# Kernel tuning notes

Hardware: AMD Instinct MI355X
Metric: run time of the kernel (lower is better)

The kernel has to match this reference:

```python
import jax, jax.numpy as jnp
import numpy as np

BS, SL, N_AGENTS, OBS_DIM, STATE_DIM, N_EDGES, HID = 32, 512, 32, 96, 1024, 64, 256


def _hgcn(w_line, x, H):
    # x: [B, n, 1]; H: [B, n, E]. Faithful to torch HGCN:
    # A = D^{-1/2} H |W| B^{-1} H^T D^{-1/2}, with D, B built from detached H/|W|,
    # inf entries (from 0^{-1} / 0^{-0.5}) zeroed. Diagonal matmuls are implicit scalings.
    w_abs = jnp.abs(w_line)
    Hd = jax.lax.stop_gradient(H)
    d = jnp.einsum('bne,e->bn', Hd, jax.lax.stop_gradient(w_abs))  # [B, n]
    d_is = jnp.where(d > 0, jax.lax.rsqrt(jnp.where(d > 0, d, 1.0)), 0.0)
    b = jnp.sum(Hd, axis=-2)  # [B, E]
    b_inv = jnp.where(b > 0, 1.0 / jnp.where(b > 0, b, 1.0), 0.0)
    t = d_is[..., None] * x                       # D^{-1/2} x
    s = jnp.einsum('bne,bnk->bek', H, t)          # H^T (...)
    s = s * (w_abs[None, :] * b_inv)[..., None]   # |W| B^{-1} (diagonals commute)
    y = jnp.einsum('bne,bek->bnk', H, s)          # H (...)
    return d_is[..., None] * y                    # D^{-1/2} (...)


def _mlp(x, w1, b1, w2, b2):
    return jax.nn.relu(x @ w1 + b1) @ w2 + b2


def setup_inputs() -> dict:
    key = jax.random.key(0)
    ks = jax.random.split(key, 24)
    f = jax.random.normal
    inp = {
        'agent_qs': f(ks[0], (BS, SL, N_AGENTS), jnp.float32),
        'states': f(ks[1], (BS, SL, STATE_DIM), jnp.float32),
        'indiv_us': f(ks[2], (BS, SL, N_AGENTS, OBS_DIM), jnp.float32),
        'edge_W': f(ks[3], (OBS_DIM, N_EDGES), jnp.float32) * 0.1,
        'edge_b': f(ks[4], (N_EDGES,), jnp.float32) * 0.1,
        'wline1': 1.0 + 0.1 * f(ks[5], (N_EDGES,), jnp.float32),
        'wline2': 1.0 + 0.1 * f(ks[6], (N_EDGES,), jnp.float32),
    }
    names = ['hw1', 'hc1', 'hw', 'hc']
    outs = [N_AGENTS, N_AGENTS, N_AGENTS, 1]
    for i, (nm, od) in enumerate(zip(names, outs)):
        inp[nm + '_w1'] = f(ks[7 + 4 * i], (STATE_DIM, HID), jnp.float32) * 0.05
        inp[nm + '_b1'] = f(ks[8 + 4 * i], (HID,), jnp.float32) * 0.05
        inp[nm + '_w2'] = f(ks[9 + 4 * i], (HID, od), jnp.float32) * 0.05
        inp[nm + '_b2'] = f(ks[10 + 4 * i], (od,), jnp.float32) * 0.05
    return inp


def reference(agent_qs, states, indiv_us, edge_W, edge_b, wline1, wline2,
              hw1_w1, hw1_b1, hw1_w2, hw1_b2, hc1_w1, hc1_b1, hc1_w2, hc1_b2,
              hw_w1, hw_b1, hw_w2, hw_b2, hc_w1, hc_b1, hc_w2, hc_b2):
    bs, sl, n = agent_qs.shape
    q = agent_qs.reshape(-1, n)                               # [B, n]
    u = indiv_us.reshape(-1, n, indiv_us.shape[-1])           # [B, n, obs]
    s = states.reshape(-1, states.shape[-1])                  # [B, state_dim]
    H = jax.nn.relu(u @ edge_W + edge_b)                      # hyper_edge_net -> [B, n, E]
    x = q[..., None]                                          # node_features [B, n, 1]
    qs_tot = _hgcn(wline2, _hgcn(wline1, x, H), H)[..., 0]    # two stacked HGCN encoders
    w1 = jnp.abs(_mlp(s, hw1_w1, hw1_b1, hw1_w2, hw1_b2))
    c1 = _mlp(s, hc1_w1, hc1_b1, hc1_w2, hc1_b2)
    qt = jax.nn.elu(qs_tot * w1 + c1)
    w = jnp.abs(_mlp(s, hw_w1, hw_b1, hw_w2, hw_b2))
    c = _mlp(s, hc_w1, hc_b1, hc_w2, hc_b2)[..., 0]
    q_tot = jnp.sum(qt * w, axis=-1) + c
    return q_tot.reshape(bs, sl, 1)
```

## Files before the change

kernel.cpp:

```cpp
#include <hip/hip_runtime.h>
#include <cstdint>

typedef _Float16 f16;
typedef _Float16 f16x2 __attribute__((ext_vector_type(2)));
typedef _Float16 f16x4 __attribute__((ext_vector_type(4)));
typedef _Float16 f16x8 __attribute__((ext_vector_type(8)));
typedef float f32x4 __attribute__((ext_vector_type(4)));

#define AS1U const __attribute__((address_space(1))) unsigned int
#define AS3U __attribute__((address_space(3))) unsigned int

__device__ __forceinline__ void gload_lds16(const void* g, void* l) {
    __builtin_amdgcn_global_load_lds((AS1U*)g, (AS3U*)l, 16, 0, 0);
}

#define WSYNC() asm volatile("s_waitcnt lgkmcnt(0)" ::: "memory")
#define CFENCE() asm volatile("" ::: "memory")

#define BATCH 16384
#define NAG   32
#define OBS   96
#define SDIM  1024
#define NE    64
#define HIDN  256
#define NH    1024

#define NB_MIX 5120
#define NB_PW  256
#define NB_SM  101
#define NB_MAIN (NB_MIX + NB_PW + NB_SM)

__global__ __launch_bounds__(256, 5) void k_main(
    const float* __restrict__ agent_qs, const float* __restrict__ states,
    const float* __restrict__ indiv_us, const float* __restrict__ edge_W,
    const float* __restrict__ edge_b, const float* __restrict__ wline1,
    const float* __restrict__ wline2,
    const float* __restrict__ w1a, const float* __restrict__ w1b,
    const float* __restrict__ w1c, const float* __restrict__ w1d,
    const float* __restrict__ b1a, const float* __restrict__ b1b,
    const float* __restrict__ b1c, const float* __restrict__ b1d,
    const float* __restrict__ w2a, const float* __restrict__ w2b,
    const float* __restrict__ w2c, const float* __restrict__ w2d,
    f16* __restrict__ states16, f16* __restrict__ W1t, float* __restrict__ b1cat,
    f16* __restrict__ W2t, f16* __restrict__ hcw2, float* __restrict__ qs_tot) {
    __shared__ __align__(16) char arena[32256];
    const int tid = threadIdx.x;
    int bid = blockIdx.x;

    if (bid < NB_MIX) {
        const int g = bid / 5, r = bid - g * 5;
        if (r == 4) {
            int i = g * 256 + tid;
            const int n4 = BATCH * SDIM / 4;
            const int stride = 1024 * 256;
            for (; i < n4; i += stride) {
                float4 v = ((const float4*)states)[i];
                f16x4 h = { (f16)v.x, (f16)v.y, (f16)v.z, (f16)v.w };
                ((f16x4*)states16)[i] = h;
            }
            return;
        }
        const int hbid = g * 4 + r;
        f16*   eWs  = (f16*)arena;
        float* swa  = (float*)(arena + 13312);
        f16*   HsB  = (f16*)(arena + 13824);
        float* svB  = (float*)(arena + 30720);
        float* sttB = (float*)(arena + 31744);

        const int w = tid >> 6, l = tid & 63;
        const int b = hbid * 4 + w;
        f16*   Hw  = HsB + w * (32 * 66);
        float* sv  = svB + w * 64;
        float* stt = sttB + w * 32;

        const int nn = l & 31, half = l >> 5;
        float q = agent_qs[(size_t)b * 32 + nn];

        for (int i = tid; i < 6144; i += 256) {
            int k = i >> 6, n = i & 63;
            eWs[n * 104 + k] = (f16)edge_W[i];
        }
        if (tid < 64) swa[tid] = fabsf(wline1[tid]);
        else if (tid < 128) swa[tid] = fabsf(wline2[tid - 64]);
        __syncthreads();

        const float swal1 = swa[l];
        const float swal2 = swa[64 + l];

        const int lm = l & 15, lk = l >> 4;
        const float* ub = indiv_us + (size_t)b * (NAG * OBS);

        #pragma unroll
        for (int mt = 0; mt < 2; mt++) {
            f16x8 af[3];
            #pragma unroll
            for (int ks = 0; ks < 3; ks++) {
                const float* up = ub + (mt * 16 + lm) * 96 + ks * 32 + lk * 8;
                float4 v0 = *(const float4*)up;
                float4 v1 = *(const float4*)(up + 4);
                af[ks] = (f16x8){ (f16)v0.x, (f16)v0.y, (f16)v0.z, (f16)v0.w,
                                  (f16)v1.x, (f16)v1.y, (f16)v1.z, (f16)v1.w };
            }
            #pragma unroll
            for (int nt = 0; nt < 4; nt++) {
                f32x4 acc = {0.f, 0.f, 0.f, 0.f};
                #pragma unroll
                for (int ks = 0; ks < 3; ks++) {
                    f16x8 bb = *(const f16x8*)&eWs[(nt * 16 + lm) * 104 + ks * 32 + lk * 8];
                    acc = __builtin_amdgcn_mfma_f32_16x16x32_f16(af[ks], bb, acc, 0, 0, 0);
                }
                int col = nt * 16 + lm;
                float bias = edge_b[col];
                #pragma unroll
                for (int r2 = 0; r2 < 4; r2++) {
                    int row = mt * 16 + lk * 4 + r2;
                    float hv = acc[r2] + bias;
                    Hw[row * 66 + col] = (f16)(hv > 0.f ? hv : 0.f);
                }
            }
        }
        WSYNC();

        float bsum = 0.f;
        #pragma unroll
        for (int n = 0; n < 32; n++) bsum += (float)Hw[n * 66 + l];
        const float sbinv_r = bsum > 0.f ? 1.f / bsum : 0.f;

        float dd = 0.f;
        #pragma unroll 8
        for (int e2 = 0; e2 < 32; e2++) {
            f16x2 h2 = *(const f16x2*)&Hw[nn * 66 + e2 * 2];
            dd += (float)h2.x * swa[half * 64 + e2 * 2] + (float)h2.y * swa[half * 64 + e2 * 2 + 1];
        }
        float dis = dd > 0.f ? rsqrtf(dd) : 0.f;
        const float dis_o = __shfl_xor(dis, 32);
        const float dis1 = (half == 0) ? dis : dis_o;
        const float dis2 = (half == 0) ? dis_o : dis;
        if (half == 0) stt[nn] = dis * q;
        WSYNC();

        float s1 = 0.f;
        #pragma unroll
        for (int n = 0; n < 32; n++) s1 += (float)Hw[n * 66 + l] * stt[n];
        sv[l] = s1 * swal1 * sbinv_r;
        WSYNC();

        float y1 = 0.f;
        #pragma unroll 8
        for (int e2 = 0; e2 < 32; e2++) {
            f16x2 h2 = *(const f16x2*)&Hw[nn * 66 + e2 * 2];
            y1 += (float)h2.x * sv[e2 * 2] + (float)h2.y * sv[e2 * 2 + 1];
        }
        float x2 = dis1 * y1;
        if (half == 0) stt[nn] = dis2 * x2;
        WSYNC();

        float s2 = 0.f;
        #pragma unroll
        for (int n = 0; n < 32; n++) s2 += (float)Hw[n * 66 + l] * stt[n];
        sv[l] = s2 * swal2 * sbinv_r;
        WSYNC();

        float y2 = 0.f;
        #pragma unroll 8
        for (int e2 = 0; e2 < 32; e2++) {
            f16x2 h2 = *(const f16x2*)&Hw[nn * 66 + e2 * 2];
            y2 += (float)h2.x * sv[e2 * 2] + (float)h2.y * sv[e2 * 2 + 1];
        }
        if (half == 0) qs_tot[(size_t)b * 32 + nn] = dis2 * y2;
        return;
    }
    bid -= NB_MIX;

    if (bid < NB_PW) {
        float* tile = (float*)arena;
        int mlp = bid >> 6, rem = bid & 63, kt = rem >> 2, ct = rem & 3;
        const float* src = (mlp == 0) ? w1a : (mlp == 1) ? w1b : (mlp == 2) ? w1c : w1d;
        int k0 = kt * 64, c0 = ct * 64;
        for (int i = tid; i < 4096; i += 256) {
            int kk = i >> 6, cc = i & 63;
            tile[kk * 65 + cc] = src[(size_t)(k0 + kk) * 256 + c0 + cc];
        }
        __syncthreads();
        for (int i = tid; i < 4096; i += 256) {
            int cc = i >> 6, kk = i & 63;
            W1t[(size_t)(mlp * 256 + c0 + cc) * 1024 + k0 + kk] = (f16)tile[kk * 65 + cc];
        }
        return;
    }
    bid -= NB_PW;
    {
        int i = bid * 256 + tid;
        if (i < 24576) {
            int mp = i >> 13, rem = i & 8191, oo = rem >> 8, kk = rem & 255;
            const float* src = (mp == 0) ? w2a : (mp == 1) ? w2b : w2c;
            W2t[i] = (f16)src[kk * 32 + oo];
        } else if (i < 24832) {
            int k = i - 24576;
            hcw2[k] = (f16)w2d[k];
        } else if (i < 25856) {
            int n = i - 24832;
            int mlp = n >> 8, c = n & 255;
            const float* bsrc = (mlp == 0) ? b1a : (mlp == 1) ? b1b : (mlp == 2) ? b1c : b1d;
            b1cat[n] = bsrc[c];
        }
    }
}

__global__ __launch_bounds__(512) void k_gemm(
    const f16* __restrict__ A, const f16* __restrict__ B,
    const float* __restrict__ b1cat, const f16* __restrict__ W2t,
    const f16* __restrict__ hcw2, float* __restrict__ Pp) {
    __shared__ __align__(16) char smem[131072];
    f16* Asb = (f16*)smem;
    f16* Bsb = (f16*)(smem + 65536);
    f16* Ts  = (f16*)smem;

    const int tid = threadIdx.x;
    const int w = tid >> 6, l = tid & 63;
    const int lm = l & 15, lk = l >> 4;
    const int wm = w >> 2, wn = w & 3;
    const int p = blockIdx.x;
    const int xcd = p & 7, s = p >> 3;
    const int mt = xcd * 8 + (s >> 2);
    const int nt = s & 3;
    const int m0 = mt * 256, n0 = nt * 256;
    const int c0 = w * 4;
    const int srow = l >> 3;
    const int gchunk = (l & 7) ^ srow;

    float bj[4];
    #pragma unroll
    for (int j = 0; j < 4; j++) bj[j] = b1cat[n0 + wn * 64 + j * 16 + lm];

    f32x4 acc[8][4];
    #pragma unroll
    for (int i = 0; i < 8; i++)
        #pragma unroll
        for (int j = 0; j < 4; j++) acc[i][j] = (f32x4){0.f, 0.f, 0.f, 0.f};

#define STAGE(KT, BI)                                                                     \
    {                                                                                     \
        f16* Ad = Asb + (BI) * 16384;                                                     \
        f16* Bd = Bsb + (BI) * 16384;                                                     \
        _Pragma("unroll")                                                                 \
        for (int i_ = 0; i_ < 4; i_++) {                                                  \
            int cc = c0 + i_;                                                             \
            gload_lds16(&A[(size_t)(m0 + cc * 8 + srow) * 1024 + (KT) * 64 + gchunk * 8], \
                        &Ad[cc * 512]);                                                   \
            gload_lds16(&B[(size_t)(n0 + cc * 8 + srow) * 1024 + (KT) * 64 + gchunk * 8], \
                        &Bd[cc * 512]);                                                   \
        }                                                                                 \
    }

    STAGE(0, 0);
    STAGE(1, 1);

    for (int kt = 0; kt < 16; kt++) {
        if (kt < 15) { asm volatile("s_waitcnt vmcnt(8)" ::: "memory"); }
        else         { asm volatile("s_waitcnt vmcnt(0)" ::: "memory"); }
        CFENCE(); __builtin_amdgcn_s_barrier(); CFENCE();

        const f16* As_ = Asb + (kt & 1) * 16384;
        const f16* Bs_ = Bsb + (kt & 1) * 16384;
        const int swlo = ((lk ^ (lm & 7)) << 3);
        const int swhi = (((4 + lk) ^ (lm & 7)) << 3);

        f16x8 af[4][2], bf01[2][2], bf23[2][2];

        #pragma unroll
        for (int i = 0; i < 4; i++) {
            af[i][0] = *(const f16x8*)&As_[(wm * 128 + i * 16 + lm) * 64 + swlo];
            af[i][1] = *(const f16x8*)&As_[(wm * 128 + i * 16 + lm) * 64 + swhi];
        }
        #pragma unroll
        for (int j = 0; j < 2; j++) {
            bf01[j][0] = *(const f16x8*)&Bs_[(wn * 64 + j * 16 + lm) * 64 + swlo];
            bf01[j][1] = *(const f16x8*)&Bs_[(wn * 64 + j * 16 + lm) * 64 + swhi];
        }
        __builtin_amdgcn_s_setprio(1);
        #pragma unroll
        for (int ks = 0; ks < 2; ks++)
            #pragma unroll
            for (int i = 0; i < 4; i++)
                #pragma unroll
                for (int j = 0; j < 2; j++)
                    acc[i][j] = __builtin_amdgcn_mfma_f32_16x16x32_f16(af[i][ks], bf01[j][ks], acc[i][j], 0, 0, 0);
        __builtin_amdgcn_s_setprio(0);
        CFENCE(); __builtin_amdgcn_s_barrier(); CFENCE();

        #pragma unroll
        for (int j = 0; j < 2; j++) {
            bf23[j][0] = *(const f16x8*)&Bs_[(wn * 64 + (2 + j) * 16 + lm) * 64 + swlo];
            bf23[j][1] = *(const f16x8*)&Bs_[(wn * 64 + (2 + j) * 16 + lm) * 64 + swhi];
        }
        __builtin_amdgcn_s_setprio(1);
        #pragma unroll
        for (int ks = 0; ks < 2; ks++)
            #pragma unroll
            for (int i = 0; i < 4; i++)
                #pragma unroll
                for (int j = 0; j < 2; j++)
                    acc[i][2 + j] = __builtin_amdgcn_mfma_f32_16x16x32_f16(af[i][ks], bf23[j][ks], acc[i][2 + j], 0, 0, 0);
        __builtin_amdgcn_s_setprio(0);
        CFENCE(); __builtin_amdgcn_s_barrier(); CFENCE();

        #pragma unroll
        for (int i = 0; i < 4; i++) {
            af[i][0] = *(const f16x8*)&As_[(wm * 128 + (4 + i) * 16 + lm) * 64 + swlo];
            af[i][1] = *(const f16x8*)&As_[(wm * 128 + (4 + i) * 16 + lm) * 64 + swhi];
        }
        __builtin_amdgcn_s_setprio(1);
        #pragma unroll
        for (int ks = 0; ks < 2; ks++)
            #pragma unroll
            for (int i = 0; i < 4; i++)
                #pragma unroll
                for (int j = 0; j < 2; j++)
                    acc[4 + i][j] = __builtin_amdgcn_mfma_f32_16x16x32_f16(af[i][ks], bf01[j][ks], acc[4 + i][j], 0, 0, 0);
        __builtin_amdgcn_s_setprio(0);
        CFENCE(); __builtin_amdgcn_s_barrier(); CFENCE();

        if (kt < 14) STAGE(kt + 2, kt & 1);
        __builtin_amdgcn_s_setprio(1);
        #pragma unroll
        for (int ks = 0; ks < 2; ks++)
            #pragma unroll
            for (int i = 0; i < 4; i++)
                #pragma unroll
                for (int j = 0; j < 2; j++)
                    acc[4 + i][2 + j] = __builtin_amdgcn_mfma_f32_16x16x32_f16(af[i][ks], bf23[j][ks], acc[4 + i][2 + j], 0, 0, 0);
        __builtin_amdgcn_s_setprio(0);
    }
#undef STAGE

    __syncthreads();

    const int mlp = nt;
    #pragma unroll
    for (int pass = 0; pass < 2; pass++) {
        if (wm == pass) {
            #pragma unroll
            for (int i = 0; i < 8; i++)
                #pragma unroll
                for (int r = 0; r < 4; r++) {
                    int rl = i * 16 + lk * 4 + r;
                    #pragma unroll
                    for (int j = 0; j < 4; j++) {
                        float v = acc[i][j][r] + bj[j];
                        Ts[rl * 264 + wn * 64 + j * 16 + lm] = (f16)(v > 0.f ? v : 0.f);
                    }
                }
        }
        __syncthreads();
        const int grow = m0 + pass * 128 + w * 16;
        if (mlp < 3) {
            const f16* wb = W2t + mlp * 8192;
            f32x4 acc2[2];
            acc2[0] = (f32x4){0, 0, 0, 0}; acc2[1] = (f32x4){0, 0, 0, 0};
            #pragma unroll
            for (int ks = 0; ks < 8; ks++) {
                f16x8 a  = *(const f16x8*)&Ts[(w * 16 + lm) * 264 + ks * 32 + lk * 8];
                f16x8 b0 = *(const f16x8*)&wb[lm * 256 + ks * 32 + lk * 8];
                f16x8 b1 = *(const f16x8*)&wb[(16 + lm) * 256 + ks * 32 + lk * 8];
                acc2[0] = __builtin_amdgcn_mfma_f32_16x16x32_f16(a, b0, acc2[0], 0, 0, 0);
                acc2[1] = __builtin_amdgcn_mfma_f32_16x16x32_f16(a, b1, acc2[1], 0, 0, 0);
            }
            #pragma unroll
            for (int j2 = 0; j2 < 2; j2++)
                #pragma unroll
                for (int r = 0; r < 4; r++)
                    Pp[(size_t)(grow + lk * 4 + r) * 104 + mlp * 32 + j2 * 16 + lm] = acc2[j2][r];
        } else {
            f32x4 acc2 = (f32x4){0, 0, 0, 0};
            #pragma unroll
            for (int ks = 0; ks < 8; ks++) {
                f16x8 a = *(const f16x8*)&Ts[(w * 16 + lm) * 264 + ks * 32 + lk * 8];
                f16x8 bz = (f16x8){0, 0, 0, 0, 0, 0, 0, 0};
                if (lm == 0) bz = *(const f16x8*)&hcw2[ks * 32 + lk * 8];
                acc2 = __builtin_amdgcn_mfma_f32_16x16x32_f16(a, bz, acc2, 0, 0, 0);
            }
            if (lm == 0)
                #pragma unroll
                for (int r = 0; r < 4; r++)
                    Pp[(size_t)(grow + lk * 4 + r) * 104 + 96] = acc2[r];
        }
        if (pass == 0) __syncthreads();
    }
}

__global__ __launch_bounds__(256) void k_ep(
    const float* __restrict__ Pp, const float* __restrict__ qs_tot,
    const float* __restrict__ hw1_b2, const float* __restrict__ hc1_b2,
    const float* __restrict__ hw_b2, const float* __restrict__ hc_b2,
    float* __restrict__ out) {
    const int tid = threadIdx.x;
    const int row = blockIdx.x * 32 + (tid >> 3);
    const int q8 = tid & 7, o = q8 * 4;
    const float* p0 = Pp + (size_t)row * 104;
    f32x4 a0 = *(const f32x4*)(p0 + o);
    f32x4 c0 = *(const f32x4*)(p0 + 32 + o);
    f32x4 w0 = *(const f32x4*)(p0 + 64 + o);
    f32x4 qs = *(const f32x4*)(qs_tot + (size_t)row * 32 + o);
    float val = 0.f;
    #pragma unroll
    for (int j = 0; j < 4; j++) {
        float wv1 = fabsf(a0[j] + hw1_b2[o + j]);
        float cv1 = c0[j] + hc1_b2[o + j];
        float wv  = fabsf(w0[j] + hw_b2[o + j]);
        float z = qs[j] * wv1 + cv1;
        float qt = z > 0.f ? z : expm1f(z);
        val += qt * wv;
    }
    val += __shfl_xor(val, 1);
    val += __shfl_xor(val, 2);
    val += __shfl_xor(val, 4);
    if (q8 == 0) out[row] = val + p0[96] + hc_b2[0];
}

extern "C" void kernel_launch(void* const* d_in, const int* in_sizes, int n_in,
                              void* d_out, int out_size, void* d_ws, size_t ws_size,
                              hipStream_t stream) {
    const float* agent_qs = (const float*)d_in[0];
    const float* states   = (const float*)d_in[1];
    const float* indiv_us = (const float*)d_in[2];
    const float* edge_W   = (const float*)d_in[3];
    const float* edge_b   = (const float*)d_in[4];
    const float* wline1   = (const float*)d_in[5];
    const float* wline2   = (const float*)d_in[6];
    const float* hw1_w1 = (const float*)d_in[7];
    const float* hw1_b1 = (const float*)d_in[8];
    const float* hw1_w2 = (const float*)d_in[9];
    const float* hw1_b2 = (const float*)d_in[10];
    const float* hc1_w1 = (const float*)d_in[11];
    const float* hc1_b1 = (const float*)d_in[12];
    const float* hc1_w2 = (const float*)d_in[13];
    const float* hc1_b2 = (const float*)d_in[14];
    const float* hw_w1  = (const float*)d_in[15];
    const float* hw_b1  = (const float*)d_in[16];
    const float* hw_w2  = (const float*)d_in[17];
    const float* hw_b2  = (const float*)d_in[18];
    const float* hc_w1  = (const float*)d_in[19];
    const float* hc_b1  = (const float*)d_in[20];
    const float* hc_w2  = (const float*)d_in[21];
    const float* hc_b2  = (const float*)d_in[22];

    char* ws = (char*)d_ws;
    size_t o_states16 = 0;
    size_t o_W1t  = o_states16 + (size_t)BATCH * SDIM * 2;
    size_t o_b1   = o_W1t + (size_t)NH * SDIM * 2;
    size_t o_W2t  = o_b1 + 4096;
    size_t o_hcw2 = o_W2t + 49152;
    size_t o_Pp   = o_hcw2 + 512;
    size_t o_qs   = o_Pp + (size_t)BATCH * 104 * 4;

    f16*   states16 = (f16*)(ws + o_states16);
    f16*   W1t      = (f16*)(ws + o_W1t);
    float* b1cat    = (float*)(ws + o_b1);
    f16*   W2t      = (f16*)(ws + o_W2t);
    f16*   hcw2     = (f16*)(ws + o_hcw2);
    float* Pp       = (float*)(ws + o_Pp);
    float* qs_tot   = (float*)(ws + o_qs);

    k_main<<<NB_MAIN, 256, 0, stream>>>(
        agent_qs, states, indiv_us, edge_W, edge_b, wline1, wline2,
        hw1_w1, hc1_w1, hw_w1, hc_w1, hw1_b1, hc1_b1, hw_b1, hc_b1,
        hw1_w2, hc1_w2, hw_w2, hc_w2,
        states16, W1t, b1cat, W2t, hcw2, qs_tot);
    k_gemm<<<256, 512, 0, stream>>>(states16, W1t, b1cat, W2t, hcw2, Pp);
    k_ep<<<BATCH / 32, 256, 0, stream>>>(Pp, qs_tot, hw1_b2, hc1_b2, hw_b2, hc_b2,
                                         (float*)d_out);
}
```

Before: 116.6 us.

## Keep hypergraph incidence matrix in MFMA registers and reduce with wave shuffles

The HGCN part no longer writes the relu'd incidence matrix H to LDS in f16. It keeps the MFMA accumulator fragments in registers as fp32 and does the degree sums, the two H^T/H products and the normalisations with cross-lane xor-shuffle reductions. This removes the per-wave LDS traffic and the lgkmcnt waits, and shrinks the shared arena, which can allow more blocks per CU. The trade is many shuffle instructions and higher register pressure. The min-blocks hint is also dropped from launch_bounds, so the compiler may pick a different occupancy.

```diff
diff --git a/kernel.cpp b/kernel.cpp
--- a/kernel.cpp
+++ b/kernel.cpp
@@ -14,7 +14,6 @@
     __builtin_amdgcn_global_load_lds((AS1U*)g, (AS3U*)l, 16, 0, 0);
 }
 
-#define WSYNC() asm volatile("s_waitcnt lgkmcnt(0)" ::: "memory")
 #define CFENCE() asm volatile("" ::: "memory")
 
 #define BATCH 16384
@@ -30,7 +29,7 @@
 #define NB_SM  101
 #define NB_MAIN (NB_MIX + NB_PW + NB_SM)
 
-__global__ __launch_bounds__(256, 5) void k_main(
+__global__ __launch_bounds__(256) void k_main(
     const float* __restrict__ agent_qs, const float* __restrict__ states,
     const float* __restrict__ indiv_us, const float* __restrict__ edge_W,
     const float* __restrict__ edge_b, const float* __restrict__ wline1,
@@ -43,13 +42,13 @@
     const float* __restrict__ w2c, const float* __restrict__ w2d,
     f16* __restrict__ states16, f16* __restrict__ W1t, float* __restrict__ b1cat,
     f16* __restrict__ W2t, f16* __restrict__ hcw2, float* __restrict__ qs_tot) {
-    __shared__ __align__(16) char arena[32256];
+    __shared__ __align__(16) char arena[16640];
     const int tid = threadIdx.x;
     int bid = blockIdx.x;
 
     if (bid < NB_MIX) {
-        const int g = bid / 5, r = bid - g * 5;
-        if (r == 4) {
+        const int g = bid / 5, r5 = bid - g * 5;
+        if (r5 == 4) {
             int i = g * 256 + tid;
             const int n4 = BATCH * SDIM / 4;
             const int stride = 1024 * 256;
@@ -60,21 +59,13 @@
             }
             return;
         }
-        const int hbid = g * 4 + r;
-        f16*   eWs  = (f16*)arena;
-        float* swa  = (float*)(arena + 13312);
-        f16*   HsB  = (f16*)(arena + 13824);
-        float* svB  = (float*)(arena + 30720);
-        float* sttB = (float*)(arena + 31744);
+        const int hbid = g * 4 + r5;
+        f16*   eWs = (f16*)arena;
+        float* swa = (float*)(arena + 13312);
 
         const int w = tid >> 6, l = tid & 63;
         const int b = hbid * 4 + w;
-        f16*   Hw  = HsB + w * (32 * 66);
-        float* sv  = svB + w * 64;
-        float* stt = sttB + w * 32;
-
-        const int nn = l & 31, half = l >> 5;
-        float q = agent_qs[(size_t)b * 32 + nn];
+        const int lm = l & 15, lk = l >> 4;
 
         for (int i = tid; i < 6144; i += 256) {
             int k = i >> 6, n = i & 63;
@@ -84,12 +75,16 @@
         else if (tid < 128) swa[tid] = fabsf(wline2[tid - 64]);
         __syncthreads();
 
-        const float swal1 = swa[l];
-        const float swal2 = swa[64 + l];
-
-        const int lm = l & 15, lk = l >> 4;
+        float sw1[4], sw2[4], eb[4];
+        #pragma unroll
+        for (int nt = 0; nt < 4; nt++) {
+            sw1[nt] = swa[nt * 16 + lm];
+            sw2[nt] = swa[64 + nt * 16 + lm];
+            eb[nt]  = edge_b[nt * 16 + lm];
+        }
+
         const float* ub = indiv_us + (size_t)b * (NAG * OBS);
-
+        f32x4 hh[2][4];
         #pragma unroll
         for (int mt = 0; mt < 2; mt++) {
             f16x8 af[3];
@@ -109,65 +104,104 @@
                     f16x8 bb = *(const f16x8*)&eWs[(nt * 16 + lm) * 104 + ks * 32 + lk * 8];
                     acc = __builtin_amdgcn_mfma_f32_16x16x32_f16(af[ks], bb, acc, 0, 0, 0);
                 }
-                int col = nt * 16 + lm;
-                float bias = edge_b[col];
-                #pragma unroll
-                for (int r2 = 0; r2 < 4; r2++) {
-                    int row = mt * 16 + lk * 4 + r2;
-                    float hv = acc[r2] + bias;
-                    Hw[row * 66 + col] = (f16)(hv > 0.f ? hv : 0.f);
+                #pragma unroll
+                for (int r = 0; r < 4; r++) {
+                    float v = acc[r] + eb[nt];
+                    hh[mt][nt][r] = v > 0.f ? v : 0.f;
                 }
             }
         }
-        WSYNC();
-
-        float bsum = 0.f;
-        #pragma unroll
-        for (int n = 0; n < 32; n++) bsum += (float)Hw[n * 66 + l];
-        const float sbinv_r = bsum > 0.f ? 1.f / bsum : 0.f;
-
-        float dd = 0.f;
-        #pragma unroll 8
-        for (int e2 = 0; e2 < 32; e2++) {
-            f16x2 h2 = *(const f16x2*)&Hw[nn * 66 + e2 * 2];
-            dd += (float)h2.x * swa[half * 64 + e2 * 2] + (float)h2.y * swa[half * 64 + e2 * 2 + 1];
-        }
-        float dis = dd > 0.f ? rsqrtf(dd) : 0.f;
-        const float dis_o = __shfl_xor(dis, 32);
-        const float dis1 = (half == 0) ? dis : dis_o;
-        const float dis2 = (half == 0) ? dis_o : dis;
-        if (half == 0) stt[nn] = dis * q;
-        WSYNC();
-
-        float s1 = 0.f;
-        #pragma unroll
-        for (int n = 0; n < 32; n++) s1 += (float)Hw[n * 66 + l] * stt[n];
-        sv[l] = s1 * swal1 * sbinv_r;
-        WSYNC();
-
-        float y1 = 0.f;
-        #pragma unroll 8
-        for (int e2 = 0; e2 < 32; e2++) {
-            f16x2 h2 = *(const f16x2*)&Hw[nn * 66 + e2 * 2];
-            y1 += (float)h2.x * sv[e2 * 2] + (float)h2.y * sv[e2 * 2 + 1];
-        }
-        float x2 = dis1 * y1;
-        if (half == 0) stt[nn] = dis2 * x2;
-        WSYNC();
-
-        float s2 = 0.f;
-        #pragma unroll
-        for (int n = 0; n < 32; n++) s2 += (float)Hw[n * 66 + l] * stt[n];
-        sv[l] = s2 * swal2 * sbinv_r;
-        WSYNC();
-
-        float y2 = 0.f;
-        #pragma unroll 8
-        for (int e2 = 0; e2 < 32; e2++) {
-            f16x2 h2 = *(const f16x2*)&Hw[nn * 66 + e2 * 2];
-            y2 += (float)h2.x * sv[e2 * 2] + (float)h2.y * sv[e2 * 2 + 1];
-        }
-        if (half == 0) qs_tot[(size_t)b * 32 + nn] = dis2 * y2;
+
+        float binv[4];
+        #pragma unroll
+        for (int nt = 0; nt < 4; nt++) {
+            float bs = 0.f;
+            #pragma unroll
+            for (int mt = 0; mt < 2; mt++)
+                #pragma unroll
+                for (int r = 0; r < 4; r++) bs += hh[mt][nt][r];
+            bs += __shfl_xor(bs, 16);
+            bs += __shfl_xor(bs, 32);
+            binv[nt] = bs > 0.f ? 1.f / bs : 0.f;
+        }
+
+        float dis1[2][4], dis2[2][4];
+        #pragma unroll
+        for (int mt = 0; mt < 2; mt++)
+            #pragma unroll
+            for (int r = 0; r < 4; r++) {
+                float a1 = 0.f, a2 = 0.f;
+                #pragma unroll
+                for (int nt = 0; nt < 4; nt++) {
+                    a1 += hh[mt][nt][r] * sw1[nt];
+                    a2 += hh[mt][nt][r] * sw2[nt];
+                }
+                a1 += __shfl_xor(a1, 1); a1 += __shfl_xor(a1, 2);
+                a1 += __shfl_xor(a1, 4); a1 += __shfl_xor(a1, 8);
+                a2 += __shfl_xor(a2, 1); a2 += __shfl_xor(a2, 2);
+                a2 += __shfl_xor(a2, 4); a2 += __shfl_xor(a2, 8);
+                dis1[mt][r] = a1 > 0.f ? rsqrtf(a1) : 0.f;
+                dis2[mt][r] = a2 > 0.f ? rsqrtf(a2) : 0.f;
+            }
+
+        float t1[2][4];
+        #pragma unroll
+        for (int mt = 0; mt < 2; mt++)
+            #pragma unroll
+            for (int r = 0; r < 4; r++)
+                t1[mt][r] = dis1[mt][r] * agent_qs[(size_t)b * 32 + mt * 16 + lk * 4 + r];
+
+        float s1s[4];
+        #pragma unroll
+        for (int nt = 0; nt < 4; nt++) {
+            float s = 0.f;
+            #pragma unroll
+            for (int mt = 0; mt < 2; mt++)
+                #pragma unroll
+                for (int r = 0; r < 4; r++) s += hh[mt][nt][r] * t1[mt][r];
+            s += __shfl_xor(s, 16);
+            s += __shfl_xor(s, 32);
+            s1s[nt] = s * sw1[nt] * binv[nt];
+        }
+
+        float t2[2][4];
+        #pragma unroll
+        for (int mt = 0; mt < 2; mt++)
+            #pragma unroll
+            for (int r = 0; r < 4; r++) {
+                float y = 0.f;
+                #pragma unroll
+                for (int nt = 0; nt < 4; nt++) y += hh[mt][nt][r] * s1s[nt];
+                y += __shfl_xor(y, 1); y += __shfl_xor(y, 2);
+                y += __shfl_xor(y, 4); y += __shfl_xor(y, 8);
+                t2[mt][r] = dis2[mt][r] * (dis1[mt][r] * y);
+            }
+
+        float s2s[4];
+        #pragma unroll
+        for (int nt = 0; nt < 4; nt++) {
+            float s = 0.f;
+            #pragma unroll
+            for (int mt = 0; mt < 2; mt++)
+                #pragma unroll
+                for (int r = 0; r < 4; r++) s += hh[mt][nt][r] * t2[mt][r];
+            s += __shfl_xor(s, 16);
+            s += __shfl_xor(s, 32);
+            s2s[nt] = s * sw2[nt] * binv[nt];
+        }
+
+        #pragma unroll
+        for (int mt = 0; mt < 2; mt++)
+            #pragma unroll
+            for (int r = 0; r < 4; r++) {
+                float y = 0.f;
+                #pragma unroll
+                for (int nt = 0; nt < 4; nt++) y += hh[mt][nt][r] * s2s[nt];
+                y += __shfl_xor(y, 1); y += __shfl_xor(y, 2);
+                y += __shfl_xor(y, 4); y += __shfl_xor(y, 8);
+                if (lm == 0)
+                    qs_tot[(size_t)b * 32 + mt * 16 + lk * 4 + r] = dis2[mt][r] * y;
+            }
         return;
     }
     bid -= NB_MIX;
```

Result: no change. 117.7 us (+1.0%).
